# Kernel tuning notes

Hardware: AMD Instinct MI355X
Metric: run time of the kernel (lower is better)

## Reference

```python
import jax, jax.numpy as jnp
import numpy as np

B, N, M = 2, 1024, 512
D, H, DH = 1024, 16, 64          # features, heads, head dim (D == H*DH)
MID = H * DH
DC = 768                          # context_features
MULT = 4
EPS = 1e-5


def _ln(x, w, b):
    mu = jnp.mean(x, -1, keepdims=True)
    var = jnp.mean((x - mu) ** 2, -1, keepdims=True)
    return (x - mu) * jax.lax.rsqrt(var + EPS) * w + b


def _sincos(n, d):
    inv = 1.0 / (10000.0 ** (jnp.arange(0, d, 2, dtype=jnp.float32) / d))
    ang = jnp.arange(n, dtype=jnp.float32)[:, None] * inv[None, :]
    return jnp.sin(ang), jnp.cos(ang)


def _rope(x, sin, cos):
    # x: [B,H,N,DH]; sin/cos: [N, DH//2]; interleaved even/odd rotation
    s = sin[None, None]
    c = cos[None, None]
    xe = x[..., ::2]
    xo = x[..., 1::2]
    re = xe * c - xo * s
    ro = xe * s + xo * c
    return jnp.stack((re, ro), axis=-1).reshape(x.shape)


def _heads(t):
    b, n, _ = t.shape
    return t.reshape(b, n, H, DH).transpose(0, 2, 1, 3)


def _attn(xq, ctx, wq, wkv, wo, bo):
    q = _heads(xq @ wq)
    k, v = jnp.split(ctx @ wkv, 2, axis=-1)
    k = _heads(k)
    v = _heads(v)
    sq, cq = _sincos(q.shape[2], DH)
    sk, ck = _sincos(k.shape[2], DH)
    q = _rope(q, sq, cq)
    k = _rope(k, sk, ck)
    sim = jnp.einsum('bhnd,bhmd->bhnm', q, k) * (DH ** -0.5)
    a = jax.nn.softmax(sim, axis=-1)
    o = jnp.einsum('bhnm,bhmd->bhnd', a, v)
    o = o.transpose(0, 2, 1, 3).reshape(xq.shape[0], xq.shape[1], MID)
    return o @ wo + bo


def _adaln(x, c, lw, lb, gw, gb, bw, bb):
    g = (c @ gw + gb)[:, None, :]
    bt = (c @ bw + bb)[:, None, :]
    return _ln(x, lw, lb) * (1.0 + g) + bt


def setup_inputs() -> dict:
    ks = jax.random.split(jax.random.key(0), 24)
    s = 0.02
    inp = {
        'x': jax.random.normal(ks[0], (B, N, D), jnp.float32),
        'cond': jax.random.normal(ks[1], (B, D), jnp.float32),
        'context': jax.random.normal(ks[2], (B, M, DC), jnp.float32),
        # AdaLN (attn_mod) — reused for self- and cross-attention pre-norm
        'ln1_w': jnp.ones((D,), jnp.float32),
        'ln1_b': jnp.zeros((D,), jnp.float32),
        'g1_w': jax.random.normal(ks[3], (D, D), jnp.float32) * s,
        'g1_b': jnp.zeros((D,), jnp.float32),
        'b1_w': jax.random.normal(ks[4], (D, D), jnp.float32) * s,
        'b1_b': jnp.zeros((D,), jnp.float32),
        # AdaLN (ffn_mod)
        'ln2_w': jnp.ones((D,), jnp.float32),
        'ln2_b': jnp.zeros((D,), jnp.float32),
        'g2_w': jax.random.normal(ks[5], (D, D), jnp.float32) * s,
        'g2_b': jnp.zeros((D,), jnp.float32),
        'b2_w': jax.random.normal(ks[6], (D, D), jnp.float32) * s,
        'b2_b': jnp.zeros((D,), jnp.float32),
        # self-attention
        'sa_wq': jax.random.normal(ks[7], (D, MID), jnp.float32) * s,
        'sa_wkv': jax.random.normal(ks[8], (D, 2 * MID), jnp.float32) * s,
        'sa_wo': jax.random.normal(ks[9], (MID, D), jnp.float32) * s,
        'sa_bo': jnp.zeros((D,), jnp.float32),
        # cross-attention (context LayerNorm + projections)
        'ca_lnc_w': jnp.ones((DC,), jnp.float32),
        'ca_lnc_b': jnp.zeros((DC,), jnp.float32),
        'ca_wq': jax.random.normal(ks[10], (D, MID), jnp.float32) * s,
        'ca_wkv': jax.random.normal(ks[11], (DC, 2 * MID), jnp.float32) * s,
        'ca_wo': jax.random.normal(ks[12], (MID, D), jnp.float32) * s,
        'ca_bo': jnp.zeros((D,), jnp.float32),
        # FFN
        'ff_w1': jax.random.normal(ks[13], (D, MULT * D), jnp.float32) * s,
        'ff_b1': jnp.zeros((MULT * D,), jnp.float32),
        'ff_w2': jax.random.normal(ks[14], (MULT * D, D), jnp.float32) * s,
        'ff_b2': jnp.zeros((D,), jnp.float32),
    }
    return inp


def reference(x, cond, context,
              ln1_w, ln1_b, g1_w, g1_b, b1_w, b1_b,
              ln2_w, ln2_b, g2_w, g2_b, b2_w, b2_b,
              sa_wq, sa_wkv, sa_wo, sa_bo,
              ca_lnc_w, ca_lnc_b, ca_wq, ca_wkv, ca_wo, ca_bo,
              ff_w1, ff_b1, ff_w2, ff_b2):
    # self-attention with shared attn_mod AdaLN
    attn_in = _adaln(x, cond, ln1_w, ln1_b, g1_w, g1_b, b1_w, b1_b)
    x = _attn(attn_in, attn_in, sa_wq, sa_wkv, sa_wo, sa_bo) + x
    # cross-attention (attn_mod reused, context LayerNorm applied)
    cross_in = _adaln(x, cond, ln1_w, ln1_b, g1_w, g1_b, b1_w, b1_b)
    ctx_n = _ln(context, ca_lnc_w, ca_lnc_b)
    x = _attn(cross_in, ctx_n, ca_wq, ca_wkv, ca_wo, ca_bo) + x
    # FFN with ffn_mod AdaLN, exact GELU (torch default)
    ffn_in = _adaln(x, cond, ln2_w, ln2_b, g2_w, g2_b, b2_w, b2_b)
    h = jax.nn.gelu(ffn_in @ ff_w1 + ff_b1, approximate=False)
    x = h @ ff_w2 + ff_b2 + x
    return x
```

## Files before the change

kernel.cpp:

```cpp
#include <hip/hip_runtime.h>
#include <hip/hip_bf16.h>
#include <math.h>


typedef float f32x4 __attribute__((ext_vector_type(4)));
typedef __bf16 bf16x8 __attribute__((ext_vector_type(8)));
typedef __bf16 bf16x4 __attribute__((ext_vector_type(4)));
typedef __bf16 bf16x2 __attribute__((ext_vector_type(2)));

#define DEVI __device__ __forceinline__

DEVI void gload16(const void* g, void* l) {
  __builtin_amdgcn_global_load_lds((const __attribute__((address_space(1))) void*)g,
                                   (__attribute__((address_space(3))) void*)l, 16, 0, 0);
}

struct WtDesc {
  const float* src[8];
  __bf16* dst[8];
  int K[8], N[8];
  int tstart[9];
};

__global__ __launch_bounds__(256) void wt_all_kernel(WtDesc d) {
  __shared__ float tile[32][33];
  int blk = blockIdx.x;
  int e = 0;
#pragma unroll
  for (int i = 0; i < 7; ++i) e += (blk >= d.tstart[i + 1]) ? 1 : 0;
  int li = blk - d.tstart[e];
  const float* W = d.src[e];
  __bf16* WT = d.dst[e];
  int K = d.K[e], N = d.N[e];
  int ntx = N >> 5;
  int n0 = (li % ntx) * 32, k0 = (li / ntx) * 32;
  int tx = threadIdx.x & 31, ty = threadIdx.x >> 5;
#pragma unroll
  for (int i = 0; i < 4; ++i) {
    int k = ty + i * 8;
    tile[k][tx] = W[(size_t)(k0 + k) * N + n0 + tx];
  }
  __syncthreads();
#pragma unroll
  for (int i = 0; i < 4; ++i) {
    int n = ty + i * 8;
    WT[(size_t)(n0 + n) * K + k0 + tx] = (__bf16)tile[tx][n];
  }
}

__global__ __launch_bounds__(256) void mod_part_kernel(
    const float* __restrict__ cond,
    const float* __restrict__ g1w, const float* __restrict__ b1w,
    const float* __restrict__ g2w, const float* __restrict__ b2w,
    float* __restrict__ part) {
  __shared__ float sc[128];
  int dchunk = blockIdx.x, b = blockIdx.y;
  int mat = blockIdx.z >> 3, ks = blockIdx.z & 7;
  const float* W = (mat == 0) ? g1w : (mat == 1) ? b1w : (mat == 2) ? g2w : b2w;
  if (threadIdx.x < 128) sc[threadIdx.x] = cond[b * 1024 + ks * 128 + threadIdx.x];
  __syncthreads();
  int d = dchunk * 256 + threadIdx.x;
  const float* Wp = W + (size_t)(ks * 128) * 1024 + d;
  float acc = 0.f;
#pragma unroll 8
  for (int k = 0; k < 128; ++k) acc += sc[k] * Wp[(size_t)k * 1024];
  part[(size_t)(blockIdx.z * 2 + b) * 1024 + d] = acc;
}

__global__ __launch_bounds__(256) void mod_reduce_kernel(
    const float* __restrict__ part,
    const float* __restrict__ g1b, const float* __restrict__ b1b,
    const float* __restrict__ g2b, const float* __restrict__ b2b,
    float* __restrict__ mods) {
  int idx = blockIdx.x * 256 + threadIdx.x;
  int mat = idx >> 11, b = (idx >> 10) & 1, d = idx & 1023;
  float s = 0.f;
#pragma unroll
  for (int ks = 0; ks < 8; ++ks) s += part[(size_t)((mat * 8 + ks) * 2 + b) * 1024 + d];
  const float* Bv = (mat == 0) ? g1b : (mat == 1) ? b1b : (mat == 2) ? g2b : b2b;
  mods[(size_t)(mat * 2 + b) * 1024 + d] = s + Bv[d];
}

__global__ __launch_bounds__(256) void adaln_kernel(const float* __restrict__ X,
                                                    const float* __restrict__ lnw,
                                                    const float* __restrict__ lnb,
                                                    const float* __restrict__ mods,
                                                    int gi, int bi,
                                                    __bf16* __restrict__ out) {
  __shared__ float red[2][4];
  int row = blockIdx.x;
  int b = row >> 10;
  int t = threadIdx.x;
  const float4 xv = ((const float4*)(X + (size_t)row * 1024))[t];
  float s  = xv.x + xv.y + xv.z + xv.w;
  float s2 = xv.x * xv.x + xv.y * xv.y + xv.z * xv.z + xv.w * xv.w;
  int lane = t & 63, w = t >> 6;
#pragma unroll
  for (int off = 32; off > 0; off >>= 1) {
    s += __shfl_down(s, off);
    s2 += __shfl_down(s2, off);
  }
  if (lane == 0) { red[0][w] = s; red[1][w] = s2; }
  __syncthreads();
  s  = red[0][0] + red[0][1] + red[0][2] + red[0][3];
  s2 = red[1][0] + red[1][1] + red[1][2] + red[1][3];
  float mu = s * (1.0f / 1024.0f);
  float var = s2 * (1.0f / 1024.0f) - mu * mu;
  float rstd = rsqrtf(var + 1e-5f);
  const float4 wv = ((const float4*)lnw)[t];
  const float4 bv = ((const float4*)lnb)[t];
  const float4 gv = ((const float4*)(mods + (size_t)(gi * 2 + b) * 1024))[t];
  const float4 tv = ((const float4*)(mods + (size_t)(bi * 2 + b) * 1024))[t];
  bf16x4 ov;
  ov[0] = (__bf16)(((xv.x - mu) * rstd * wv.x + bv.x) * (1.0f + gv.x) + tv.x);
  ov[1] = (__bf16)(((xv.y - mu) * rstd * wv.y + bv.y) * (1.0f + gv.y) + tv.y);
  ov[2] = (__bf16)(((xv.z - mu) * rstd * wv.z + bv.z) * (1.0f + gv.z) + tv.z);
  ov[3] = (__bf16)(((xv.w - mu) * rstd * wv.w + bv.w) * (1.0f + gv.w) + tv.w);
  *(bf16x4*)(out + (size_t)row * 1024 + t * 4) = ov;
}

__global__ __launch_bounds__(256) void ctxln_kernel(const float* __restrict__ X,
                                                    const float* __restrict__ w,
                                                    const float* __restrict__ bias,
                                                    __bf16* __restrict__ out) {
  __shared__ float red[2][4];
  int row = blockIdx.x;
  int t = threadIdx.x;
  const float* xp = X + (size_t)row * 768;
  float v[3];
  float s = 0.f, s2 = 0.f;
#pragma unroll
  for (int i = 0; i < 3; ++i) {
    v[i] = xp[t + i * 256];
    s += v[i];
    s2 += v[i] * v[i];
  }
  int lane = t & 63, wv_ = t >> 6;
#pragma unroll
  for (int off = 32; off > 0; off >>= 1) {
    s += __shfl_down(s, off);
    s2 += __shfl_down(s2, off);
  }
  if (lane == 0) { red[0][wv_] = s; red[1][wv_] = s2; }
  __syncthreads();
  s  = red[0][0] + red[0][1] + red[0][2] + red[0][3];
  s2 = red[1][0] + red[1][1] + red[1][2] + red[1][3];
  float mu = s * (1.0f / 768.0f);
  float var = s2 * (1.0f / 768.0f) - mu * mu;
  float rstd = rsqrtf(var + 1e-5f);
#pragma unroll
  for (int i = 0; i < 3; ++i) {
    int c = t + i * 256;
    out[(size_t)row * 768 + c] = (__bf16)((v[i] - mu) * rstd * w[c] + bias[c]);
  }
}

__global__ __launch_bounds__(256) void rope_tbl_kernel(float2* __restrict__ tbl) {
  int idx = blockIdx.x * 256 + threadIdx.x;
  int n = idx >> 5, i = idx & 31;
  float inv = expf(-(float)(2 * i) * (1.0f / 64.0f) * 9.210340371976184f);
  float ang = (float)n * inv;
  tbl[idx] = make_float2(sinf(ang), cosf(ang));
}

__global__ __launch_bounds__(256) void rope_kernel(const float* __restrict__ X, int ldx, int col0,
                                                   const float2* __restrict__ tbl,
                                                   __bf16* __restrict__ out, int Ntok, float scale) {
  int idx = blockIdx.x * 256 + threadIdx.x;
  int i = idx & 31;
  int h = (idx >> 5) & 15;
  int nn = idx >> 9;
  int n = nn % Ntok;
  int b = nn / Ntok;
  const float* xp = X + (size_t)(b * Ntok + n) * ldx + col0 + h * 64 + 2 * i;
  float xe = xp[0], xo = xp[1];
  float2 sc2 = tbl[n * 32 + i];
  float re = (xe * sc2.y - xo * sc2.x) * scale;
  float ro = (xe * sc2.x + xo * sc2.y) * scale;
  __bf16* op = out + ((size_t)(b * 16 + h) * Ntok + n) * 64 + 2 * i;
  op[0] = (__bf16)re;
  op[1] = (__bf16)ro;
}

__global__ __launch_bounds__(256) void vt_kernel(const float* __restrict__ KV, int ld, int col0,
                                                 __bf16* __restrict__ VT, int Ntok) {
  __shared__ float tile[32][33];
  int bh = blockIdx.x;
  int n0 = blockIdx.y * 32, d0 = blockIdx.z * 32;
  int b = bh >> 4, h = bh & 15;
  int tx = threadIdx.x & 31, ty = threadIdx.x >> 5;
#pragma unroll
  for (int i = 0; i < 4; ++i) {
    int n = ty + i * 8;
    tile[n][tx] = KV[(size_t)(b * Ntok + n0 + n) * ld + col0 + h * 64 + d0 + tx];
  }
  __syncthreads();
#pragma unroll
  for (int i = 0; i < 4; ++i) {
    int d = ty + i * 8;
    VT[((size_t)bh * 64 + d0 + d) * Ntok + n0 + tx] = (__bf16)tile[tx][d];
  }
}

template <int BM, int BN, int EPI, int DEPTH>
__global__ __launch_bounds__(256) void gemm3(const __bf16* __restrict__ A,
                                             const __bf16* __restrict__ BT,
                                             const float* __restrict__ bias,
                                             const float* __restrict__ res,
                                             void* __restrict__ outv,
                                             int M, int N, int K, int kslices) {
  constexpr int MI = BM / 32, NI = BN / 32;
  constexpr int NBUF = DEPTH + 1;
  constexpr int LPT = BM / 64 + BN / 64;
  __shared__ __bf16 sA[NBUF][BM * 32];
  __shared__ __bf16 sB[NBUF][BN * 32];
  const int t = threadIdx.x;
  const int w = t >> 6, lane = t & 63;
  const int lr = lane & 15, lg = lane >> 4;
  const int fxor = (lr >> 1) & 3;
  int nwg = gridDim.x * gridDim.y * gridDim.z;
  int flat = blockIdx.x + gridDim.x * (blockIdx.y + gridDim.y * blockIdx.z);
  flat = (flat & 7) * (nwg >> 3) + (flat >> 3);
  const int bm = flat % gridDim.x;
  int rest = flat / gridDim.x;
  const int bn = rest % gridDim.y;
  const int bz = rest / gridDim.y;
  const int wm = (w >> 1) * (BM / 2), wn = (w & 1) * (BN / 2);
  const int kper = K / kslices;
  const int k0 = bz * kper;
  const int nsteps = kper / 32;
  f32x4 acc[MI][NI] = {};

  auto stage = [&](int buf, int kt) {
#pragma unroll
    for (int i = 0; i < BM / 64; ++i) {
      int e8 = i * 256 + t;
      int row = e8 >> 2, c = e8 & 3;
      int scol = (c ^ ((row >> 1) & 3)) << 3;
      gload16(A + (size_t)(bm * BM + row) * K + kt + scol, &sA[buf][e8 * 8]);
    }
#pragma unroll
    for (int i = 0; i < BN / 64; ++i) {
      int e8 = i * 256 + t;
      int row = e8 >> 2, c = e8 & 3;
      int scol = (c ^ ((row >> 1) & 3)) << 3;
      gload16(BT + (size_t)(bn * BN + row) * K + kt + scol, &sB[buf][e8 * 8]);
    }
  };

  auto compute = [&](int buf) {
    bf16x8 af[MI], bfr[NI];
#pragma unroll
    for (int mi = 0; mi < MI; ++mi)
      af[mi] = *(const bf16x8*)(&sA[buf][(wm + mi * 16 + lr) * 32 + ((lg ^ fxor) << 3)]);
#pragma unroll
    for (int ni = 0; ni < NI; ++ni)
      bfr[ni] = *(const bf16x8*)(&sB[buf][(wn + ni * 16 + lr) * 32 + ((lg ^ fxor) << 3)]);
#pragma unroll
    for (int mi = 0; mi < MI; ++mi)
#pragma unroll
      for (int ni = 0; ni < NI; ++ni)
        acc[mi][ni] = __builtin_amdgcn_mfma_f32_16x16x32_bf16(af[mi], bfr[ni], acc[mi][ni], 0, 0, 0);
  };

#pragma unroll
  for (int i = 0; i < DEPTH; ++i) stage(i, k0 + i * 32);

  int it = 0;
  for (; it < nsteps - (DEPTH - 1); ++it) {
    asm volatile("s_waitcnt vmcnt(%0)" :: "n"((DEPTH - 1) * LPT) : "memory");
    __builtin_amdgcn_s_barrier();
    __builtin_amdgcn_sched_barrier(0);
    if (it + DEPTH < nsteps) stage((it + DEPTH) % NBUF, k0 + (it + DEPTH) * 32);
    compute(it % NBUF);
  }
  asm volatile("s_waitcnt vmcnt(0)" ::: "memory");
  __builtin_amdgcn_s_barrier();
  __builtin_amdgcn_sched_barrier(0);
  for (; it < nsteps; ++it) compute(it % NBUF);

#pragma unroll
  for (int mi = 0; mi < MI; ++mi) {
    int row = bm * BM + wm + mi * 16 + lg * 4;
#pragma unroll
    for (int ni = 0; ni < NI; ++ni) {
      int col = bn * BN + wn + ni * 16 + lr;
#pragma unroll
      for (int r = 0; r < 4; ++r) {
        float v = acc[mi][ni][r];
        size_t off = (size_t)(row + r) * N + col;
        if (EPI == 0) {
          ((float*)outv)[off] = v;
        } else if (EPI == 1) {
          ((float*)outv)[off] = v + bias[col] + res[off];
        } else if (EPI == 2) {
          float xg = v + bias[col];
          ((__bf16*)outv)[off] = (__bf16)(0.5f * xg * (1.0f + erff(xg * 0.7071067811865475f)));
        } else {
          ((float*)outv)[(size_t)bz * M * N + off] = v;
        }
      }
    }
  }
}

__global__ __launch_bounds__(256) void ff2red_kernel(const float* __restrict__ part,
                                                     const float* __restrict__ bias,
                                                     const float* __restrict__ res,
                                                     float* __restrict__ out, int MN, int N) {
  int idx = blockIdx.x * 256 + threadIdx.x;
  float4 p0 = ((const float4*)part)[idx];
  float4 p1 = ((const float4*)(part + MN))[idx];
  float4 rr = ((const float4*)res)[idx];
  int colb = (idx * 4) & (N - 1);
  float4 bb = *(const float4*)(bias + colb);
  float4 o;
  o.x = p0.x + p1.x + bb.x + rr.x;
  o.y = p0.y + p1.y + bb.y + rr.y;
  o.z = p0.z + p1.z + bb.z + rr.z;
  o.w = p0.w + p1.w + bb.w + rr.w;
  ((float4*)out)[idx] = o;
}

template <int KITERS>
__global__ __launch_bounds__(256) void attn_part_kernel(const __bf16* __restrict__ Qr,
                                                        const __bf16* __restrict__ Kr,
                                                        const __bf16* __restrict__ VT,
                                                        float* __restrict__ pO,
                                                        float* __restrict__ pml,
                                                        int Nq, int Nk) {
  __shared__ __bf16 sK[2][64 * 64];
  __shared__ __bf16 sV[2][64 * 64];
  __shared__ __bf16 Pl[4][16 * 64];
  const int t = threadIdx.x, w = t >> 6, lane = t & 63;
  const int lr = lane & 15, lg = lane >> 4;
  const int lsrc = lane & 48;
  const int swz = (lr & 7) << 3;
  int flat = blockIdx.x + (blockIdx.y << 4) + (blockIdx.z << 9);
  flat = (flat & 7) * 128 + (flat >> 3);
  const int bh = (flat >> 4) & 31, z = flat >> 9;
  const int q0 = (flat & 15) * 64 + w * 16;
  const int k0 = z * (KITERS * 64);

  auto stage = [&](int buf, int kt) {
#pragma unroll
    for (int i = 0; i < 2; ++i) {
      int e8 = i * 256 + t;
      int row = e8 >> 3, col8 = e8 & 7;
      int scol = (col8 ^ (row & 7)) << 3;
      gload16(Kr + ((size_t)bh * Nk + kt + row) * 64 + scol, &sK[buf][e8 * 8]);
      gload16(VT + ((size_t)bh * 64 + row) * Nk + kt + scol, &sV[buf][e8 * 8]);
    }
  };

  bf16x8 qf[2];
#pragma unroll
  for (int kh = 0; kh < 2; ++kh)
    qf[kh] = *(const bf16x8*)(Qr + ((size_t)bh * Nq + q0 + lr) * 64 + kh * 32 + lg * 8);
  f32x4 accO[4] = {};
  float m = -INFINITY, l = 0.f;

  stage(0, k0);
  __syncthreads();
  int cur = 0;
#pragma unroll
  for (int it = 0; it < KITERS; ++it) {
    if (it + 1 < KITERS) stage(cur ^ 1, k0 + (it + 1) * 64);
    f32x4 s[4] = {};
#pragma unroll
    for (int nf = 0; nf < 4; ++nf) {
      int r = nf * 16 + lr;
#pragma unroll
      for (int kh = 0; kh < 2; ++kh) {
        bf16x8 kf = *(const bf16x8*)(&sK[cur][r * 64 + (((kh * 4 + lg) ^ (lr & 7)) << 3)]);
        s[nf] = __builtin_amdgcn_mfma_f32_16x16x32_bf16(kf, qf[kh], s[nf], 0, 0, 0);
      }
    }
    float p[16];
#pragma unroll
    for (int j = 0; j < 16; ++j) p[j] = s[j >> 2][j & 3];
    float pm = p[0];
#pragma unroll
    for (int j = 1; j < 16; ++j) pm = fmaxf(pm, p[j]);
    pm = fmaxf(pm, __shfl_xor(pm, 16));
    pm = fmaxf(pm, __shfl_xor(pm, 32));
    if (!__all(pm <= m + 8.f)) {
      float mnew = fmaxf(m, pm);
      float resc = __expf(m - mnew);
      float rq[4];
#pragma unroll
      for (int r = 0; r < 4; ++r) rq[r] = __shfl(resc, lsrc | (lg * 4 + r));
#pragma unroll
      for (int df = 0; df < 4; ++df)
#pragma unroll
        for (int r = 0; r < 4; ++r) accO[df][r] *= rq[r];
      l *= resc;
      m = mnew;
    }
    float rs = 0.f;
#pragma unroll
    for (int j = 0; j < 16; ++j) { p[j] = __expf(p[j] - m); rs += p[j]; }
    rs += __shfl_xor(rs, 16);
    rs += __shfl_xor(rs, 32);
    l += rs;
#pragma unroll
    for (int nf = 0; nf < 4; ++nf)
#pragma unroll
      for (int jj = 0; jj < 2; ++jj) {
        int k = nf * 16 + lg * 4 + 2 * jj;
        bf16x2 pk;
        pk[0] = (__bf16)p[nf * 4 + 2 * jj];
        pk[1] = (__bf16)p[nf * 4 + 2 * jj + 1];
        *(bf16x2*)(&Pl[w][lr * 64 + (k ^ swz)]) = pk;
      }
    bf16x8 pa0 = *(const bf16x8*)(&Pl[w][lr * 64 + ((lg * 8) ^ swz)]);
    bf16x8 pa1 = *(const bf16x8*)(&Pl[w][lr * 64 + ((32 + lg * 8) ^ swz)]);
#pragma unroll
    for (int df = 0; df < 4; ++df) {
      int d = df * 16 + lr;
      bf16x8 vf0 = *(const bf16x8*)(&sV[cur][d * 64 + ((lg ^ (lr & 7)) << 3)]);
      bf16x8 vf1 = *(const bf16x8*)(&sV[cur][d * 64 + (((4 + lg) ^ (lr & 7)) << 3)]);
      accO[df] = __builtin_amdgcn_mfma_f32_16x16x32_bf16(pa0, vf0, accO[df], 0, 0, 0);
      accO[df] = __builtin_amdgcn_mfma_f32_16x16x32_bf16(pa1, vf1, accO[df], 0, 0, 0);
    }
    __syncthreads();
    cur ^= 1;
  }
  const size_t rbase = (size_t)(z * 32 + bh) * Nq + q0;
  if (lg == 0) {
    pml[(rbase + lr) * 2] = m;
    pml[(rbase + lr) * 2 + 1] = l;
  }
#pragma unroll
  for (int r = 0; r < 4; ++r)
#pragma unroll
    for (int df = 0; df < 4; ++df)
      pO[(rbase + lg * 4 + r) * 64 + df * 16 + lr] = accO[df][r];
}

__global__ __launch_bounds__(256) void attn_combine_kernel(const float* __restrict__ pO,
                                                           const float* __restrict__ pml,
                                                           __bf16* __restrict__ O) {
  int idx = blockIdx.x * 256 + threadIdx.x;
  int r = idx >> 6, dh = idx & 63;
  float m0 = pml[2 * r], l0 = pml[2 * r + 1];
  float m1 = pml[2 * (r + 32768)], l1 = pml[2 * (r + 32768) + 1];
  float O0 = pO[(size_t)r * 64 + dh];
  float O1 = pO[((size_t)r + 32768) * 64 + dh];
  float mm = fmaxf(m0, m1);
  float w0 = __expf(m0 - mm), w1 = __expf(m1 - mm);
  float val = (O0 * w0 + O1 * w1) / (l0 * w0 + l1 * w1);
  int bh = r >> 10, n = r & 1023;
  int b = bh >> 4, h = bh & 15;
  O[(size_t)(b * 1024 + n) * 1024 + h * 64 + dh] = (__bf16)val;
}

extern "C" void kernel_launch(void* const* d_in, const int* in_sizes, int n_in,
                              void* d_out, int out_size, void* d_ws, size_t ws_size,
                              hipStream_t stream) {
  (void)in_sizes; (void)n_in; (void)out_size; (void)ws_size;
  const float* x       = (const float*)d_in[0];
  const float* cond    = (const float*)d_in[1];
  const float* ctx     = (const float*)d_in[2];
  const float* ln1_w   = (const float*)d_in[3];
  const float* ln1_b   = (const float*)d_in[4];
  const float* g1_w    = (const float*)d_in[5];
  const float* g1_b    = (const float*)d_in[6];
  const float* b1_w    = (const float*)d_in[7];
  const float* b1_b    = (const float*)d_in[8];
  const float* ln2_w   = (const float*)d_in[9];
  const float* ln2_b   = (const float*)d_in[10];
  const float* g2_w    = (const float*)d_in[11];
  const float* g2_b    = (const float*)d_in[12];
  const float* b2_w    = (const float*)d_in[13];
  const float* b2_b    = (const float*)d_in[14];
  const float* sa_wq   = (const float*)d_in[15];
  const float* sa_wkv  = (const float*)d_in[16];
  const float* sa_wo   = (const float*)d_in[17];
  const float* sa_bo   = (const float*)d_in[18];
  const float* ca_lnc_w = (const float*)d_in[19];
  const float* ca_lnc_b = (const float*)d_in[20];
  const float* ca_wq   = (const float*)d_in[21];
  const float* ca_wkv  = (const float*)d_in[22];
  const float* ca_wo   = (const float*)d_in[23];
  const float* ca_bo   = (const float*)d_in[24];
  const float* ff_w1   = (const float*)d_in[25];
  const float* ff_b1   = (const float*)d_in[26];
  const float* ff_w2   = (const float*)d_in[27];
  const float* ff_b2   = (const float*)d_in[28];
  float* out = (float*)d_out;

  char* ws = (char*)d_ws;
  size_t o = 0;
  auto alloc = [&](size_t bytes) {
    void* p = ws + o;
    o += (bytes + 255) & ~(size_t)255;
    return p;
  };

  __bf16* wqT   = (__bf16*)alloc(1024ull * 1024 * 2);
  __bf16* wkvT  = (__bf16*)alloc(2048ull * 1024 * 2);
  __bf16* woT   = (__bf16*)alloc(1024ull * 1024 * 2);
  __bf16* cwqT  = (__bf16*)alloc(1024ull * 1024 * 2);
  __bf16* cwkvT = (__bf16*)alloc(2048ull * 768 * 2);
  __bf16* cwoT  = (__bf16*)alloc(1024ull * 1024 * 2);
  __bf16* ff1T  = (__bf16*)alloc(4096ull * 1024 * 2);
  __bf16* ff2T  = (__bf16*)alloc(1024ull * 4096 * 2);
  float*  mods  = (float*)alloc(4ull * 2 * 1024 * 4);
  float2* tbl   = (float2*)alloc(1024ull * 32 * 8);
  __bf16* ain   = (__bf16*)alloc(2048ull * 1024 * 2);
  float*  Qf    = (float*)alloc(2048ull * 1024 * 4);
  float*  KVf   = (float*)alloc(2048ull * 2048 * 4);
  __bf16* ctxn  = (__bf16*)alloc(1024ull * 768 * 2);
  __bf16* Qr    = (__bf16*)alloc(2048ull * 1024 * 2);
  __bf16* Kr    = (__bf16*)alloc(2048ull * 1024 * 2);
  __bf16* VTb   = (__bf16*)alloc(2048ull * 1024 * 2);
  __bf16* Ob    = (__bf16*)alloc(2048ull * 1024 * 2);
  float*  x1    = (float*)alloc(2048ull * 1024 * 4);
  float*  x2    = (float*)alloc(2048ull * 1024 * 4);
  float*  QKVf  = Qf;
  __bf16* hb    = (__bf16*)KVf;
  float*  pbuf  = (float*)Qr;
  float*  mpart = (float*)Qf;
  float*  pO    = (float*)KVf;
  float*  pml   = (float*)Qf;

  WtDesc wd;
  const float* srcs[8] = {sa_wq, sa_wkv, sa_wo, ca_wq, ca_wkv, ca_wo, ff_w1, ff_w2};
  __bf16* dsts[8] = {wqT, wkvT, woT, cwqT, cwkvT, cwoT, ff1T, ff2T};
  int Ks[8] = {1024, 1024, 1024, 1024, 768, 1024, 1024, 4096};
  int Ns[8] = {1024, 2048, 1024, 1024, 2048, 1024, 4096, 1024};
  int cum = 0;
  for (int i = 0; i < 8; ++i) {
    wd.src[i] = srcs[i]; wd.dst[i] = dsts[i]; wd.K[i] = Ks[i]; wd.N[i] = Ns[i];
    wd.tstart[i] = cum;
    cum += (Ks[i] >> 5) * (Ns[i] >> 5);
  }
  wd.tstart[8] = cum;
  wt_all_kernel<<<cum, 256, 0, stream>>>(wd);
  rope_tbl_kernel<<<128, 256, 0, stream>>>(tbl);
  mod_part_kernel<<<dim3(4, 2, 32), 256, 0, stream>>>(cond, g1_w, b1_w, g2_w, b2_w, mpart);
  mod_reduce_kernel<<<32, 256, 0, stream>>>(mpart, g1_b, b1_b, g2_b, b2_b, mods);

  adaln_kernel<<<2048, 256, 0, stream>>>(x, ln1_w, ln1_b, mods, 0, 1, ain);
  gemm3<128, 128, 0, 3><<<dim3(16, 24), 256, 0, stream>>>(ain, wqT, nullptr, nullptr, QKVf, 2048, 3072, 1024, 1);
  rope_kernel<<<4096, 256, 0, stream>>>(QKVf, 3072, 0, tbl, Qr, 1024, 0.125f);
  rope_kernel<<<4096, 256, 0, stream>>>(QKVf, 3072, 1024, tbl, Kr, 1024, 1.0f);
  vt_kernel<<<dim3(32, 32, 2), 256, 0, stream>>>(QKVf, 3072, 2048, VTb, 1024);
  attn_part_kernel<8><<<dim3(16, 32, 2), 256, 0, stream>>>(Qr, Kr, VTb, pO, pml, 1024, 1024);
  attn_combine_kernel<<<8192, 256, 0, stream>>>(pO, pml, Ob);
  gemm3<128, 64, 1, 5><<<dim3(16, 16), 256, 0, stream>>>(Ob, woT, sa_bo, x, x1, 2048, 1024, 1024, 1);

  adaln_kernel<<<2048, 256, 0, stream>>>(x1, ln1_w, ln1_b, mods, 0, 1, ain);
  ctxln_kernel<<<1024, 256, 0, stream>>>(ctx, ca_lnc_w, ca_lnc_b, ctxn);
  gemm3<128, 64, 0, 5><<<dim3(16, 16), 256, 0, stream>>>(ain, cwqT, nullptr, nullptr, Qf, 2048, 1024, 1024, 1);
  gemm3<128, 64, 0, 5><<<dim3(8, 32), 256, 0, stream>>>(ctxn, cwkvT, nullptr, nullptr, KVf, 1024, 2048, 768, 1);
  rope_kernel<<<4096, 256, 0, stream>>>(Qf, 1024, 0, tbl, Qr, 1024, 0.125f);
  rope_kernel<<<2048, 256, 0, stream>>>(KVf, 2048, 0, tbl, Kr, 512, 1.0f);
  vt_kernel<<<dim3(32, 16, 2), 256, 0, stream>>>(KVf, 2048, 1024, VTb, 512);
  attn_part_kernel<4><<<dim3(16, 32, 2), 256, 0, stream>>>(Qr, Kr, VTb, pO, pml, 1024, 512);
  attn_combine_kernel<<<8192, 256, 0, stream>>>(pO, pml, Ob);
  gemm3<128, 64, 1, 5><<<dim3(16, 16), 256, 0, stream>>>(Ob, cwoT, ca_bo, x1, x2, 2048, 1024, 1024, 1);

  adaln_kernel<<<2048, 256, 0, stream>>>(x2, ln2_w, ln2_b, mods, 2, 3, ain);
  gemm3<128, 128, 2, 3><<<dim3(16, 32), 256, 0, stream>>>(ain, ff1T, ff_b1, nullptr, hb, 2048, 4096, 1024, 1);
  gemm3<128, 64, 3, 5><<<dim3(16, 16, 2), 256, 0, stream>>>(hb, ff2T, nullptr, nullptr, pbuf, 2048, 1024, 4096, 2);
  ff2red_kernel<<<2048, 256, 0, stream>>>(pbuf, ff_b2, x2, out, 2048 * 1024, 1024);
}
```

Before: 289.0 us.

## Fuse RoPE into QKV GEMM epilogues and drop split-K attention combine

The QKV and cross-attention Q/KV GEMMs now apply RoPE, the 1/8 scale and the head layout in their epilogues, writing bf16 Q/K and a bf16 V buffer directly. The separate fp32 round trip and rope kernels go away, and V is transposed from bf16 by a wider-vector kernel. Attention no longer splits over keys into partials plus a combine kernel; each block runs the full key range and normalizes in place. GEMM pipeline depth also drops from 5 to 3 for the 128x64 tiles. The trade-off is half as many attention blocks, so less parallelism, in exchange for fewer launches and less memory traffic.

```diff
diff --git a/kernel.cpp b/kernel.cpp
--- a/kernel.cpp
+++ b/kernel.cpp
@@ -163,42 +163,28 @@
   tbl[idx] = make_float2(sinf(ang), cosf(ang));
 }
 
-__global__ __launch_bounds__(256) void rope_kernel(const float* __restrict__ X, int ldx, int col0,
-                                                   const float2* __restrict__ tbl,
-                                                   __bf16* __restrict__ out, int Ntok, float scale) {
-  int idx = blockIdx.x * 256 + threadIdx.x;
-  int i = idx & 31;
-  int h = (idx >> 5) & 15;
-  int nn = idx >> 9;
-  int n = nn % Ntok;
-  int b = nn / Ntok;
-  const float* xp = X + (size_t)(b * Ntok + n) * ldx + col0 + h * 64 + 2 * i;
-  float xe = xp[0], xo = xp[1];
-  float2 sc2 = tbl[n * 32 + i];
-  float re = (xe * sc2.y - xo * sc2.x) * scale;
-  float ro = (xe * sc2.x + xo * sc2.y) * scale;
-  __bf16* op = out + ((size_t)(b * 16 + h) * Ntok + n) * 64 + 2 * i;
-  op[0] = (__bf16)re;
-  op[1] = (__bf16)ro;
-}
-
-__global__ __launch_bounds__(256) void vt_kernel(const float* __restrict__ KV, int ld, int col0,
-                                                 __bf16* __restrict__ VT, int Ntok) {
-  __shared__ float tile[32][33];
-  int bh = blockIdx.x;
-  int n0 = blockIdx.y * 32, d0 = blockIdx.z * 32;
+__global__ __launch_bounds__(256) void vtb_kernel(const __bf16* __restrict__ Vb,
+                                                  __bf16* __restrict__ VT, int Ntok) {
+  __shared__ __bf16 tile[64][68];
+  int bh = blockIdx.x, nt = blockIdx.y;
   int b = bh >> 4, h = bh & 15;
-  int tx = threadIdx.x & 31, ty = threadIdx.x >> 5;
+  int t = threadIdx.x;
+  int tx = t & 15, ty = t >> 4;
 #pragma unroll
   for (int i = 0; i < 4; ++i) {
-    int n = ty + i * 8;
-    tile[n][tx] = KV[(size_t)(b * Ntok + n0 + n) * ld + col0 + h * 64 + d0 + tx];
+    int n = ty + i * 16;
+    bf16x4 v = *(const bf16x4*)(Vb + (size_t)(b * Ntok + nt * 64 + n) * 1024 + h * 64 + tx * 4);
+#pragma unroll
+    for (int j = 0; j < 4; ++j) tile[n][tx * 4 + j] = v[j];
   }
   __syncthreads();
 #pragma unroll
   for (int i = 0; i < 4; ++i) {
-    int d = ty + i * 8;
-    VT[((size_t)bh * 64 + d0 + d) * Ntok + n0 + tx] = (__bf16)tile[tx][d];
+    int d = ty + i * 16;
+    bf16x4 o;
+#pragma unroll
+    for (int j = 0; j < 4; ++j) o[j] = tile[tx * 4 + j][d];
+    *(bf16x4*)(VT + ((size_t)bh * 64 + d) * Ntok + nt * 64 + tx * 4) = o;
   }
 }
 
@@ -208,7 +194,12 @@
                                              const float* __restrict__ bias,
                                              const float* __restrict__ res,
                                              void* __restrict__ outv,
-                                             int M, int N, int K, int kslices) {
+                                             int M, int N, int K, int kslices,
+                                             const float2* __restrict__ tbl,
+                                             __bf16* __restrict__ Qro,
+                                             __bf16* __restrict__ Kro,
+                                             __bf16* __restrict__ Vbo,
+                                             int Ntok) {
   constexpr int MI = BM / 32, NI = BN / 32;
   constexpr int NBUF = DEPTH + 1;
   constexpr int LPT = BM / 64 + BN / 64;
@@ -288,7 +279,8 @@
 #pragma unroll
       for (int r = 0; r < 4; ++r) {
         float v = acc[mi][ni][r];
-        size_t off = (size_t)(row + r) * N + col;
+        int erow = row + r;
+        size_t off = (size_t)erow * N + col;
         if (EPI == 0) {
           ((float*)outv)[off] = v;
         } else if (EPI == 1) {
@@ -296,8 +288,39 @@
         } else if (EPI == 2) {
           float xg = v + bias[col];
           ((__bf16*)outv)[off] = (__bf16)(0.5f * xg * (1.0f + erff(xg * 0.7071067811865475f)));
+        } else if (EPI == 3) {
+          ((float*)outv)[(size_t)bz * M * N + off] = v;
+        } else if (EPI == 4) {
+          float ov = __shfl_xor(v, 1);
+          int b = erow >> 10, n = erow & 1023;
+          if (col < 2048) {
+            int h = (col >> 6) & 15, dh = col & 63;
+            float2 sc = tbl[n * 32 + (dh >> 1)];
+            float rv = (lr & 1) ? (ov * sc.x + v * sc.y) : (v * sc.y - ov * sc.x);
+            __bf16* dst;
+            if (col < 1024) { rv *= 0.125f; dst = Qro; } else dst = Kro;
+            dst[((size_t)(b * 16 + h) * Ntok + n) * 64 + dh] = (__bf16)rv;
+          } else {
+            Vbo[(size_t)erow * 1024 + (col - 2048)] = (__bf16)v;
+          }
+        } else if (EPI == 5) {
+          float ov = __shfl_xor(v, 1);
+          int b = erow >> 10, n = erow & 1023;
+          int h = col >> 6, dh = col & 63;
+          float2 sc = tbl[n * 32 + (dh >> 1)];
+          float rv = ((lr & 1) ? (ov * sc.x + v * sc.y) : (v * sc.y - ov * sc.x)) * 0.125f;
+          Qro[((size_t)(b * 16 + h) * Ntok + n) * 64 + dh] = (__bf16)rv;
         } else {
-          ((float*)outv)[(size_t)bz * M * N + off] = v;
+          float ov = __shfl_xor(v, 1);
+          int b = erow >> 9, n = erow & 511;
+          if (col < 1024) {
+            int h = col >> 6, dh = col & 63;
+            float2 sc = tbl[n * 32 + (dh >> 1)];
+            float rv = (lr & 1) ? (ov * sc.x + v * sc.y) : (v * sc.y - ov * sc.x);
+            Kro[((size_t)(b * 16 + h) * Ntok + n) * 64 + dh] = (__bf16)rv;
+          } else {
+            Vbo[(size_t)erow * 1024 + (col - 1024)] = (__bf16)v;
+          }
         }
       }
     }
@@ -323,12 +346,11 @@
 }
 
 template <int KITERS>
-__global__ __launch_bounds__(256) void attn_part_kernel(const __bf16* __restrict__ Qr,
-                                                        const __bf16* __restrict__ Kr,
-                                                        const __bf16* __restrict__ VT,
-                                                        float* __restrict__ pO,
-                                                        float* __restrict__ pml,
-                                                        int Nq, int Nk) {
+__global__ __launch_bounds__(256) void attn_kernel(const __bf16* __restrict__ Qr,
+                                                   const __bf16* __restrict__ Kr,
+                                                   const __bf16* __restrict__ VT,
+                                                   __bf16* __restrict__ O,
+                                                   int Nq, int Nk) {
   __shared__ __bf16 sK[2][64 * 64];
   __shared__ __bf16 sV[2][64 * 64];
   __shared__ __bf16 Pl[4][16 * 64];
@@ -336,11 +358,11 @@
   const int lr = lane & 15, lg = lane >> 4;
   const int lsrc = lane & 48;
   const int swz = (lr & 7) << 3;
-  int flat = blockIdx.x + (blockIdx.y << 4) + (blockIdx.z << 9);
-  flat = (flat & 7) * 128 + (flat >> 3);
-  const int bh = (flat >> 4) & 31, z = flat >> 9;
+  int flat = blockIdx.x + (blockIdx.y << 4);
+  flat = (flat & 7) * 64 + (flat >> 3);
+  const int bh = flat >> 4;
   const int q0 = (flat & 15) * 64 + w * 16;
-  const int k0 = z * (KITERS * 64);
+  const int b = bh >> 4, h = bh & 15;
 
   auto stage = [&](int buf, int kt) {
 #pragma unroll
@@ -360,12 +382,12 @@
   f32x4 accO[4] = {};
   float m = -INFINITY, l = 0.f;
 
-  stage(0, k0);
+  stage(0, 0);
   __syncthreads();
   int cur = 0;
 #pragma unroll
   for (int it = 0; it < KITERS; ++it) {
-    if (it + 1 < KITERS) stage(cur ^ 1, k0 + (it + 1) * 64);
+    if (it + 1 < KITERS) stage(cur ^ 1, (it + 1) * 64);
     f32x4 s[4] = {};
 #pragma unroll
     for (int nf = 0; nf < 4; ++nf) {
@@ -426,33 +448,17 @@
     __syncthreads();
     cur ^= 1;
   }
-  const size_t rbase = (size_t)(z * 32 + bh) * Nq + q0;
-  if (lg == 0) {
-    pml[(rbase + lr) * 2] = m;
-    pml[(rbase + lr) * 2 + 1] = l;
-  }
-#pragma unroll
-  for (int r = 0; r < 4; ++r)
+  float lq[4];
+#pragma unroll
+  for (int r = 0; r < 4; ++r) lq[r] = __shfl(l, lsrc | (lg * 4 + r));
+#pragma unroll
+  for (int r = 0; r < 4; ++r) {
+    float inv = 1.0f / lq[r];
+    int n = q0 + lg * 4 + r;
 #pragma unroll
     for (int df = 0; df < 4; ++df)
-      pO[(rbase + lg * 4 + r) * 64 + df * 16 + lr] = accO[df][r];
-}
-
-__global__ __launch_bounds__(256) void attn_combine_kernel(const float* __restrict__ pO,
-                                                           const float* __restrict__ pml,
-                                                           __bf16* __restrict__ O) {
-  int idx = blockIdx.x * 256 + threadIdx.x;
-  int r = idx >> 6, dh = idx & 63;
-  float m0 = pml[2 * r], l0 = pml[2 * r + 1];
-  float m1 = pml[2 * (r + 32768)], l1 = pml[2 * (r + 32768) + 1];
-  float O0 = pO[(size_t)r * 64 + dh];
-  float O1 = pO[((size_t)r + 32768) * 64 + dh];
-  float mm = fmaxf(m0, m1);
-  float w0 = __expf(m0 - mm), w1 = __expf(m1 - mm);
-  float val = (O0 * w0 + O1 * w1) / (l0 * w0 + l1 * w1);
-  int bh = r >> 10, n = r & 1023;
-  int b = bh >> 4, h = bh & 15;
-  O[(size_t)(b * 1024 + n) * 1024 + h * 64 + dh] = (__bf16)val;
+      O[(size_t)(b * 1024 + n) * 1024 + h * 64 + df * 16 + lr] = (__bf16)(accO[df][r] * inv);
+  }
 }
 
 extern "C" void kernel_launch(void* const* d_in, const int* in_sizes, int n_in,
@@ -518,12 +524,10 @@
   __bf16* Ob    = (__bf16*)alloc(2048ull * 1024 * 2);
   float*  x1    = (float*)alloc(2048ull * 1024 * 4);
   float*  x2    = (float*)alloc(2048ull * 1024 * 4);
-  float*  QKVf  = Qf;
   __bf16* hb    = (__bf16*)KVf;
   float*  pbuf  = (float*)Qr;
   float*  mpart = (float*)Qf;
-  float*  pO    = (float*)KVf;
-  float*  pml   = (float*)Qf;
+  __bf16* Vb    = (__bf16*)Qf;
 
   WtDesc wd;
   const float* srcs[8] = {sa_wq, sa_wkv, sa_wo, ca_wq, ca_wkv, ca_wo, ff_w1, ff_w2};
@@ -543,27 +547,28 @@
   mod_reduce_kernel<<<32, 256, 0, stream>>>(mpart, g1_b, b1_b, g2_b, b2_b, mods);
 
   adaln_kernel<<<2048, 256, 0, stream>>>(x, ln1_w, ln1_b, mods, 0, 1, ain);
-  gemm3<128, 128, 0, 3><<<dim3(16, 24), 256, 0, stream>>>(ain, wqT, nullptr, nullptr, QKVf, 2048, 3072, 1024, 1);
-  rope_kernel<<<4096, 256, 0, stream>>>(QKVf, 3072, 0, tbl, Qr, 1024, 0.125f);
-  rope_kernel<<<4096, 256, 0, stream>>>(QKVf, 3072, 1024, tbl, Kr, 1024, 1.0f);
-  vt_kernel<<<dim3(32, 32, 2), 256, 0, stream>>>(QKVf, 3072, 2048, VTb, 1024);
-  attn_part_kernel<8><<<dim3(16, 32, 2), 256, 0, stream>>>(Qr, Kr, VTb, pO, pml, 1024, 1024);
-  attn_combine_kernel<<<8192, 256, 0, stream>>>(pO, pml, Ob);
-  gemm3<128, 64, 1, 5><<<dim3(16, 16), 256, 0, stream>>>(Ob, woT, sa_bo, x, x1, 2048, 1024, 1024, 1);
+  gemm3<128, 128, 4, 3><<<dim3(16, 24), 256, 0, stream>>>(ain, wqT, nullptr, nullptr, nullptr,
+                                                          2048, 3072, 1024, 1, tbl, Qr, Kr, Vb, 1024);
+  vtb_kernel<<<dim3(32, 16), 256, 0, stream>>>(Vb, VTb, 1024);
+  attn_kernel<16><<<dim3(16, 32), 256, 0, stream>>>(Qr, Kr, VTb, Ob, 1024, 1024);
+  gemm3<128, 64, 1, 3><<<dim3(16, 16), 256, 0, stream>>>(Ob, woT, sa_bo, x, x1,
+                                                         2048, 1024, 1024, 1, nullptr, nullptr, nullptr, nullptr, 0);
 
   adaln_kernel<<<2048, 256, 0, stream>>>(x1, ln1_w, ln1_b, mods, 0, 1, ain);
   ctxln_kernel<<<1024, 256, 0, stream>>>(ctx, ca_lnc_w, ca_lnc_b, ctxn);
-  gemm3<128, 64, 0, 5><<<dim3(16, 16), 256, 0, stream>>>(ain, cwqT, nullptr, nullptr, Qf, 2048, 1024, 1024, 1);
-  gemm3<128, 64, 0, 5><<<dim3(8, 32), 256, 0, stream>>>(ctxn, cwkvT, nullptr, nullptr, KVf, 1024, 2048, 768, 1);
-  rope_kernel<<<4096, 256, 0, stream>>>(Qf, 1024, 0, tbl, Qr, 1024, 0.125f);
-  rope_kernel<<<2048, 256, 0, stream>>>(KVf, 2048, 0, tbl, Kr, 512, 1.0f);
-  vt_kernel<<<dim3(32, 16, 2), 256, 0, stream>>>(KVf, 2048, 1024, VTb, 512);
-  attn_part_kernel<4><<<dim3(16, 32, 2), 256, 0, stream>>>(Qr, Kr, VTb, pO, pml, 1024, 512);
-  attn_combine_kernel<<<8192, 256, 0, stream>>>(pO, pml, Ob);
-  gemm3<128, 64, 1, 5><<<dim3(16, 16), 256, 0, stream>>>(Ob, cwoT, ca_bo, x1, x2, 2048, 1024, 1024, 1);
+  gemm3<128, 64, 5, 3><<<dim3(16, 16), 256, 0, stream>>>(ain, cwqT, nullptr, nullptr, nullptr,
+                                                         2048, 1024, 1024, 1, tbl, Qr, nullptr, nullptr, 1024);
+  gemm3<128, 64, 6, 3><<<dim3(8, 32), 256, 0, stream>>>(ctxn, cwkvT, nullptr, nullptr, nullptr,
+                                                        1024, 2048, 768, 1, tbl, nullptr, Kr, Vb, 512);
+  vtb_kernel<<<dim3(32, 8), 256, 0, stream>>>(Vb, VTb, 512);
+  attn_kernel<8><<<dim3(16, 32), 256, 0, stream>>>(Qr, Kr, VTb, Ob, 1024, 512);
+  gemm3<128, 64, 1, 3><<<dim3(16, 16), 256, 0, stream>>>(Ob, cwoT, ca_bo, x1, x2,
+                                                         2048, 1024, 1024, 1, nullptr, nullptr, nullptr, nullptr, 0);
 
   adaln_kernel<<<2048, 256, 0, stream>>>(x2, ln2_w, ln2_b, mods, 2, 3, ain);
-  gemm3<128, 128, 2, 3><<<dim3(16, 32), 256, 0, stream>>>(ain, ff1T, ff_b1, nullptr, hb, 2048, 4096, 1024, 1);
-  gemm3<128, 64, 3, 5><<<dim3(16, 16, 2), 256, 0, stream>>>(hb, ff2T, nullptr, nullptr, pbuf, 2048, 1024, 4096, 2);
+  gemm3<128, 128, 2, 3><<<dim3(16, 32), 256, 0, stream>>>(ain, ff1T, ff_b1, nullptr, hb,
+                                                          2048, 4096, 1024, 1, nullptr, nullptr, nullptr, nullptr, 0);
+  gemm3<128, 64, 3, 3><<<dim3(16, 16, 2), 256, 0, stream>>>(hb, ff2T, nullptr, nullptr, pbuf,
+                                                            2048, 1024, 4096, 2, nullptr, nullptr, nullptr, nullptr, 0);
   ff2red_kernel<<<2048, 256, 0, stream>>>(pbuf, ff_b2, x2, out, 2048 * 1024, 1024);
 }
```

New measurement: 272.1 us. 1.06x faster.
